# Kernel tuning notes

Measured on AMD Instinct MI355X. Metric: run time of the kernel, lower is better.

## Reference

```python
import jax, jax.numpy as jnp
import numpy as np

B, A, C_CLS = 64, 9, 20
H_FEAT, W_FEAT = 28, 28
IN_DIM, HID = 1280, 128
N_GT, M_POS = 40, 2048
AC5 = 5 * A + C_CLS


def setup_inputs() -> dict:
    key = jax.random.key(0)
    ks = jax.random.split(key, 10)
    features = jax.random.normal(ks[0], (B, IN_DIM, H_FEAT, W_FEAT), jnp.float32)
    # valid GT boxes in feature-map coordinates: (x1, y1, x2, y2, class)
    x1 = jax.random.uniform(ks[1], (B, N_GT), minval=0.0, maxval=W_FEAT - 6.0)
    y1 = jax.random.uniform(ks[2], (B, N_GT), minval=0.0, maxval=H_FEAT - 6.0)
    bw = jax.random.uniform(ks[3], (B, N_GT), minval=1.0, maxval=5.0)
    bh = jax.random.uniform(ks[4], (B, N_GT), minval=1.0, maxval=5.0)
    cls = jax.random.randint(ks[5], (B, N_GT), 0, C_CLS).astype(jnp.float32)
    bboxes = jnp.stack([x1, y1, x1 + bw, y1 + bh, cls], axis=-1)
    n_anchors_total = B * A * H_FEAT * W_FEAT
    pos_anchor_idx = jax.random.randint(ks[6], (M_POS,), 0, n_anchors_total, dtype=jnp.int32)
    neg_anchor_idx = jax.random.randint(ks[7], (M_POS,), 0, n_anchors_total, dtype=jnp.int32)
    W1 = jax.random.normal(ks[8], (HID, IN_DIM), jnp.float32) * 0.02
    b1 = jnp.zeros((HID,), jnp.float32)
    W2 = jax.random.normal(ks[9], (AC5, HID), jnp.float32) * 0.02
    b2 = jnp.zeros((AC5,), jnp.float32)
    anc = jnp.array([[1.0, 1], [2, 2], [3, 3], [4, 4], [5, 5], [2, 3], [3, 2], [3, 5], [5, 3]], jnp.float32)
    return dict(features=features, bboxes=bboxes, pos_anchor_idx=pos_anchor_idx,
                neg_anchor_idx=neg_anchor_idx, W1=W1, b1=b1, W2=W2, b2=b2, anc=anc)


def _detector_loss(features, bboxes, pos_idx, neg_idx, W1, b1, W2, b2, anc):
    Bx, _, Hf, Wf = features.shape
    N = bboxes.shape[1]
    Mp = pos_idx.shape[0]
    # ---- prediction network: two 1x1 convs (dropout skipped: eval mode) ----
    h = jnp.einsum('bchw,oc->bohw', features, W1) + b1[None, :, None, None]
    h = jax.nn.leaky_relu(h, 0.01)
    x = jnp.einsum('bchw,oc->bohw', h, W2) + b2[None, :, None, None]
    x_anchor = x[:, :5 * A].reshape(Bx, A, 5, Hf, Wf)  # (B,A,5,H,W)
    x_class = x[:, 5 * A:]                              # (B,C,H,W)
    # ---- GenerateGrid + GenerateAnchor ----
    xs = jnp.arange(Wf, dtype=jnp.float32) + 0.5
    ys = jnp.arange(Hf, dtype=jnp.float32) + 0.5
    gx, gy = jnp.meshgrid(xs, ys, indexing='xy')        # both (H,W)
    grid = jnp.stack([gx, gy], axis=-1)                 # (H,W,2)
    half = anc / 2.0                                    # (A,2)
    tl = grid[None] - half[:, None, None]               # (A,H,W,2)
    br = grid[None] + half[:, None, None]
    anchors = jnp.concatenate([tl, br], axis=-1)        # (A,H,W,4)
    p = jnp.broadcast_to(anchors[None], (Bx, A, Hf, Wf, 4)).reshape(Bx, -1, 4)  # (B,M,4)
    # ---- IoU matrix (B, M, N), exactly as source (signed w*h -> positive area) ----
    area_p = ((p[..., 0] - p[..., 2]) * (p[..., 1] - p[..., 3]))[:, :, None]
    area_b = ((bboxes[..., 2] - bboxes[..., 0]) * (bboxes[..., 3] - bboxes[..., 1]))[:, None, :]
    ix1 = jnp.maximum(p[:, :, None, 0], bboxes[:, None, :, 0])
    iy1 = jnp.maximum(p[:, :, None, 1], bboxes[:, None, :, 1])
    ix2 = jnp.minimum(p[:, :, None, 2], bboxes[:, None, :, 2])
    iy2 = jnp.minimum(p[:, :, None, 3], bboxes[:, None, :, 3])
    inter = jnp.clip(ix2 - ix1, 0.0) * jnp.clip(iy2 - iy1, 0.0)
    iou_mat = inter / (area_p + area_b - inter)          # (B,M,N)
    # ---- gather-based anchor/class extraction ----
    anc_data = jnp.transpose(x_anchor, (0, 1, 3, 4, 2)).reshape(-1, 5)  # (B*A*H*W, 5)
    pos_a = anc_data[pos_idx]
    neg_a = anc_data[neg_idx]
    conf_scores = jax.nn.sigmoid(jnp.concatenate([pos_a[:, 0], neg_a[:, 0]])[:, None])  # (2M,1)
    off = pos_a[:, 1:]
    offsets = jnp.concatenate([jax.nn.sigmoid(off[:, :2]) - 0.5, off[:, 2:]], axis=1)   # (M,4)
    cls_all = jnp.transpose(x_class, (0, 2, 3, 1))                       # (B,H,W,C)
    cls_all = jnp.broadcast_to(cls_all[:, None], (Bx, A, Hf, Wf, C_CLS)).reshape(-1, C_CLS)
    class_scores = cls_all[pos_idx]                                      # (M,C)
    # ---- match positives to GT via IoU argmax, build GT offsets/classes ----
    Mflat = A * Hf * Wf
    bpos = pos_idx // Mflat
    mpos = pos_idx % Mflat
    iou_pos = iou_mat[bpos, mpos]                 # (M,N)
    matched = jnp.argmax(iou_pos, axis=1)         # (M,)
    gt_box = bboxes[bpos, matched]                # (M,5)
    a_box = p[bpos, mpos]                         # (M,4)
    xa = 0.5 * (a_box[:, 0] + a_box[:, 2]); ya = 0.5 * (a_box[:, 1] + a_box[:, 3])
    wa = a_box[:, 2] - a_box[:, 0];          ha = a_box[:, 3] - a_box[:, 1]
    xb = 0.5 * (gt_box[:, 0] + gt_box[:, 2]); yb = 0.5 * (gt_box[:, 1] + gt_box[:, 3])
    wb = gt_box[:, 2] - gt_box[:, 0];          hb = gt_box[:, 3] - gt_box[:, 1]
    gt_offsets = jnp.stack([xb - xa, yb - ya, jnp.log(wb / wa), jnp.log(hb / ha)], axis=1)
    gt_offsets = jax.lax.stop_gradient(gt_offsets)
    gt_cls = gt_box[:, 4].astype(jnp.int32)
    # ---- losses (w_conf = w_reg = w_cls = 1) ----
    gt_conf = jnp.concatenate([jnp.ones((Mp, 1), jnp.float32), jnp.zeros((Mp, 1), jnp.float32)], axis=0)
    conf_loss = jnp.sum((conf_scores - gt_conf) ** 2) / (2.0 * Mp)
    reg_loss = jnp.sum((offsets - gt_offsets) ** 2) / Mp
    logp = jax.nn.log_softmax(class_scores, axis=-1)
    cls_loss = -jnp.mean(jnp.take_along_axis(logp, gt_cls[:, None], axis=1))
    return conf_loss + reg_loss + cls_loss


def reference(features, bboxes, pos_anchor_idx, neg_anchor_idx, W1, b1, W2, b2, anc):
    return _detector_loss(features, bboxes, pos_anchor_idx, neg_anchor_idx, W1, b1, W2, b2, anc)
```

## Files before the change

kernel.cpp:

```cpp
#include <hip/hip_runtime.h>
#include <math.h>

#define NPOS   2048
#define NANCH  4096
#define CIN    1280
#define HID    128
#define W_     28
#define HW_    784
#define AHW    7056
#define FB     (CIN*HW_)
#define SLAB   8
#define SLABF  (SLAB*HW_)
#define SLABP  6400

__device__ __forceinline__ float sigmoidf_(float x) {
    return 1.0f / (1.0f + __expf(-x));
}
__device__ __forceinline__ unsigned short f2bf(float x) {
    unsigned int u = __float_as_uint(x);
    return (unsigned short)((u + 0x7fffu + ((u >> 16) & 1u)) >> 16);
}
__device__ __forceinline__ float bf_lo(unsigned int w) { return __uint_as_float(w << 16); }
__device__ __forceinline__ float bf_hi(unsigned int w) { return __uint_as_float(w & 0xffff0000u); }

typedef __attribute__((address_space(3))) float lds_f;
typedef __attribute__((address_space(1))) const float glb_f;
__device__ __forceinline__ void gload16(const float* g, float* l) {
    __builtin_amdgcn_global_load_lds((glb_f*)g, (lds_f*)l, 16, 0, 0);
}

__global__ __launch_bounds__(256, 2) void k_fused(
    const float* __restrict__ F, const float* __restrict__ W1,
    const int* __restrict__ posi, const int* __restrict__ negi,
    unsigned short* __restrict__ Hp, int kchunk, int nslab)
{
    __shared__ float Pl[2][SLABP];
    __shared__ float Wl[2][SLAB][4][32];
    __shared__ float Gl[SLAB][128];
    __shared__ int   hwl[128];
    __shared__ int   gll[128];
    __shared__ int   nbL;

    const int b    = blockIdx.x;
    const int ks   = blockIdx.y;
    const int t    = threadIdx.x;
    const int w    = t >> 6;
    const int lane = t & 63;

    if (t == 0) nbL = 0;
    if (t < 128) hwl[t] = 0;
    __syncthreads();
#pragma unroll
    for (int r = 0; r < 16; ++r) {
        const int g    = r * 256 + t;
        const int aidx = (g < NPOS) ? posi[g] : negi[g - NPOS];
        const int bb   = aidx / AHW;
        if (bb == b) {
            const int hw   = (aidx - bb * AHW) % HW_;
            const int slot = atomicAdd(&nbL, 1);
            if (slot < 128) { hwl[slot] = hw; gll[slot] = g; }
        }
    }
    __syncthreads();
    const int nb = nbL;

    const bool wact = (w * 32) < nb;
    const int  i2   = lane >> 1;
    const int  hh   = lane & 1;
    const int  s_g  = w * 32 + i2;
    const int  a0   = w * 32 + (lane & 15) * 2;
    const int  og   = lane >> 4;

    float4 acc[2][8];
#pragma unroll
    for (int ai = 0; ai < 2; ++ai)
#pragma unroll
        for (int j = 0; j < 8; ++j) acc[ai][j] = make_float4(0.f, 0.f, 0.f, 0.f);

    const int kb0 = ks * kchunk;
    const int o_w = t >> 1, q_w = t & 1;

    {
        const float* src = F + (size_t)b * FB + (size_t)kb0 * HW_;
        for (int c = w; c < 24; c += 4)
            gload16(src + c * 256 + lane * 4, &Pl[0][c * 256]);
        if (w == 0 && lane < 32)
            gload16(src + 6144 + lane * 4, &Pl[0][6144]);
        const float4 wv = *(const float4*)&W1[(size_t)o_w * CIN + kb0 + 4 * q_w];
        Wl[0][4 * q_w + 0][o_w >> 5][o_w & 31] = wv.x;
        Wl[0][4 * q_w + 1][o_w >> 5][o_w & 31] = wv.y;
        Wl[0][4 * q_w + 2][o_w >> 5][o_w & 31] = wv.z;
        Wl[0][4 * q_w + 3][o_w >> 5][o_w & 31] = wv.w;
    }
    __syncthreads();

    int cur = 0;
    for (int sl = 0; sl < nslab; ++sl) {
        if (sl + 1 < nslab) {
            const int kb = kb0 + (sl + 1) * SLAB;
            const float* src = F + (size_t)b * FB + (size_t)kb * HW_;
            float* dst = &Pl[cur ^ 1][0];
            for (int c = w; c < 24; c += 4)
                gload16(src + c * 256 + lane * 4, dst + c * 256);
            if (w == 0 && lane < 32)
                gload16(src + 6144 + lane * 4, dst + 6144);
            const float4 wv = *(const float4*)&W1[(size_t)o_w * CIN + kb + 4 * q_w];
            Wl[cur ^ 1][4 * q_w + 0][o_w >> 5][o_w & 31] = wv.x;
            Wl[cur ^ 1][4 * q_w + 1][o_w >> 5][o_w & 31] = wv.y;
            Wl[cur ^ 1][4 * q_w + 2][o_w >> 5][o_w & 31] = wv.z;
            Wl[cur ^ 1][4 * q_w + 3][o_w >> 5][o_w & 31] = wv.w;
        }
        if (wact) {
            const int hw = hwl[s_g];
#pragma unroll
            for (int c = 0; c < 4; ++c)
                Gl[4 * hh + c][s_g] = Pl[cur][(4 * hh + c) * HW_ + hw];
#pragma unroll
            for (int kk = 0; kk < SLAB; ++kk) {
                const float2 g2 = *(const float2*)&Gl[kk][a0];
#pragma unroll
                for (int j = 0; j < 8; ++j) {
                    const float4 wv = *(const float4*)&Wl[cur][kk][og][4 * j];
                    acc[0][j].x = fmaf(g2.x, wv.x, acc[0][j].x);
                    acc[0][j].y = fmaf(g2.x, wv.y, acc[0][j].y);
                    acc[0][j].z = fmaf(g2.x, wv.z, acc[0][j].z);
                    acc[0][j].w = fmaf(g2.x, wv.w, acc[0][j].w);
                    acc[1][j].x = fmaf(g2.y, wv.x, acc[1][j].x);
                    acc[1][j].y = fmaf(g2.y, wv.y, acc[1][j].y);
                    acc[1][j].z = fmaf(g2.y, wv.z, acc[1][j].z);
                    acc[1][j].w = fmaf(g2.y, wv.w, acc[1][j].w);
                }
            }
        }
        __syncthreads();
        cur ^= 1;
    }

    if (wact) {
#pragma unroll
        for (int ai = 0; ai < 2; ++ai) {
            const int s = a0 + ai;
            if (s < nb) {
                const int g = gll[s];
                unsigned short* dst = Hp + ((size_t)ks * NANCH + g) * HID + og * 32;
                unsigned int u[16];
#pragma unroll
                for (int j = 0; j < 8; ++j) {
                    u[2 * j]     = (unsigned)f2bf(acc[ai][j].x) |
                                   ((unsigned)f2bf(acc[ai][j].y) << 16);
                    u[2 * j + 1] = (unsigned)f2bf(acc[ai][j].z) |
                                   ((unsigned)f2bf(acc[ai][j].w) << 16);
                }
#pragma unroll
                for (int q = 0; q < 4; ++q)
                    *(uint4*)(dst + 8 * q) =
                        make_uint4(u[4 * q], u[4 * q + 1], u[4 * q + 2], u[4 * q + 3]);
            }
        }
    }
}

__global__ __launch_bounds__(256) void k_loss(
    const unsigned short* __restrict__ Hp, const float* __restrict__ b1,
    int ksel, const float* __restrict__ W2, const float* __restrict__ b2,
    const int* __restrict__ posi, const int* __restrict__ negi,
    const float* __restrict__ bboxes, const float* __restrict__ anc,
    float* __restrict__ contrib)
{
    const int wid  = threadIdx.x >> 6;
    const int lane = threadIdx.x & 63;
    const int g    = blockIdx.x * 4 + wid;

    const int aidx = (g < NPOS) ? posi[g] : negi[g - NPOS];
    const int b   = aidx / AHW;
    const int rem = aidx - b * AHW;
    const int a   = rem / HW_;
    const int hw  = rem - a * HW_;
    const int hh  = hw / W_;
    const int ww  = hw - hh * W_;

    float hx = b1[2 * lane], hy = b1[2 * lane + 1];
    for (int ks = 0; ks < ksel; ++ks) {
        const unsigned raw =
            *(const unsigned*)&Hp[((size_t)ks * NANCH + g) * HID + 2 * lane];
        hx += bf_lo(raw);
        hy += bf_hi(raw);
    }
    hx = (hx > 0.0f) ? hx : 0.01f * hx;
    hy = (hy > 0.0f) ? hy : 0.01f * hy;

    if (g < NPOS) {
        float outv[25];
#pragma unroll
        for (int j = 0; j < 25; ++j) {
            const int row = (j < 5) ? (5 * a + j) : (40 + j);
            const float2 w = *(const float2*)&W2[(size_t)row * HID + 2 * lane];
            float v = fmaf(w.x, hx, w.y * hy);
#pragma unroll
            for (int off = 1; off < 64; off <<= 1) v += __shfl_xor(v, off, 64);
            outv[j] = v + b2[row];
        }

        const float wa = anc[2 * a], ha = anc[2 * a + 1];
        const float cx = ww + 0.5f, cy = hh + 0.5f;
        const float ax1 = cx - 0.5f * wa, ay1 = cy - 0.5f * ha;
        const float ax2 = cx + 0.5f * wa, ay2 = cy + 0.5f * ha;
        const float areap = wa * ha;

        float v; int vi = lane;
        if (lane < 40) {
            const float* bb = &bboxes[(size_t)(b * 40 + lane) * 5];
            const float bx1 = bb[0], by1 = bb[1], bx2 = bb[2], by2 = bb[3];
            const float areab = (bx2 - bx1) * (by2 - by1);
            const float ix1 = fmaxf(ax1, bx1), iy1 = fmaxf(ay1, by1);
            const float ix2 = fminf(ax2, bx2), iy2 = fminf(ay2, by2);
            const float inter = fmaxf(ix2 - ix1, 0.0f) * fmaxf(iy2 - iy1, 0.0f);
            v = inter / (areap + areab - inter);
        } else {
            v = -1.0f;
        }
#pragma unroll
        for (int off = 1; off < 64; off <<= 1) {
            const float ov = __shfl_xor(v, off, 64);
            const int   oi = __shfl_xor(vi, off, 64);
            if (ov > v || (ov == v && oi < vi)) { v = ov; vi = oi; }
        }
        const int m = vi;

        const float* gt = &bboxes[(size_t)(b * 40 + m) * 5];
        const float gx1 = gt[0], gy1 = gt[1], gx2 = gt[2], gy2 = gt[3];
        const int   gcls = (int)gt[4];
        const float xb = 0.5f * (gx1 + gx2), yb = 0.5f * (gy1 + gy2);
        const float wb = gx2 - gx1, hb = gy2 - gy1;
        const float go0 = xb - cx, go1 = yb - cy;
        const float go2 = __logf(wb / wa), go3 = __logf(hb / ha);

        const float o0 = sigmoidf_(outv[1]) - 0.5f;
        const float o1 = sigmoidf_(outv[2]) - 0.5f;
        const float o2 = outv[3], o3 = outv[4];
        const float reg = (o0 - go0) * (o0 - go0) + (o1 - go1) * (o1 - go1) +
                          (o2 - go2) * (o2 - go2) + (o3 - go3) * (o3 - go3);

        const float conf = sigmoidf_(outv[0]);
        const float conft = (conf - 1.0f) * (conf - 1.0f);

        float mx = outv[5];
#pragma unroll
        for (int c = 1; c < 20; ++c) mx = fmaxf(mx, outv[5 + c]);
        float se = 0.0f;
#pragma unroll
        for (int c = 0; c < 20; ++c) se += __expf(outv[5 + c] - mx);
        float lgt = 0.0f;
#pragma unroll
        for (int c = 0; c < 20; ++c) if (c == gcls) lgt = outv[5 + c];
        const float clst = -(lgt - mx - __logf(se));

        if (lane == 0)
            contrib[g] = conft * (1.0f / 4096.0f) + reg * (1.0f / 2048.0f) +
                         clst * (1.0f / 2048.0f);
    } else {
        const int row = 5 * a;
        const float2 w = *(const float2*)&W2[(size_t)row * HID + 2 * lane];
        float v = fmaf(w.x, hx, w.y * hy);
#pragma unroll
        for (int off = 1; off < 64; off <<= 1) v += __shfl_xor(v, off, 64);
        const float conf = sigmoidf_(v + b2[row]);
        if (lane == 0) contrib[g] = conf * conf * (1.0f / 4096.0f);
    }
}

__global__ __launch_bounds__(256) void k_final(const float* __restrict__ contrib,
                                               float* __restrict__ out)
{
    __shared__ float red[256];
    const int t = threadIdx.x;
    float s = 0.0f;
    for (int i = t; i < NANCH; i += 256) s += contrib[i];
    red[t] = s;
    __syncthreads();
    for (int st = 128; st > 0; st >>= 1) {
        if (t < st) red[t] += red[t + st];
        __syncthreads();
    }
    if (t == 0) out[0] = red[0];
}

extern "C" void kernel_launch(void* const* d_in, const int* in_sizes, int n_in,
                              void* d_out, int out_size, void* d_ws, size_t ws_size,
                              hipStream_t stream)
{
    const float* F      = (const float*)d_in[0];
    const float* bboxes = (const float*)d_in[1];
    const int*   posi   = (const int*)d_in[2];
    const int*   negi   = (const int*)d_in[3];
    const float* W1     = (const float*)d_in[4];
    const float* b1     = (const float*)d_in[5];
    const float* W2     = (const float*)d_in[6];
    const float* b2     = (const float*)d_in[7];
    const float* anc    = (const float*)d_in[8];
    float* out = (float*)d_out;

    char* ws = (char*)d_ws;
    int KSEL = 4;
    {
        const int opts[2] = {8, 4};
        for (int i = 0; i < 2; ++i) {
            size_t need = (size_t)opts[i] * NANCH * HID * 2 + (size_t)NANCH * 4 + 256;
            if (need <= ws_size) { KSEL = opts[i]; break; }
        }
    }
    unsigned short* Hp      = (unsigned short*)ws;
    float*          contrib = (float*)(ws + (size_t)KSEL * NANCH * HID * 2);

    const int kchunk = CIN / KSEL;
    const int nslab  = kchunk / SLAB;

    k_fused<<<dim3(64, KSEL), 256, 0, stream>>>(F, W1, posi, negi, Hp,
                                                kchunk, nslab);
    k_loss<<<NANCH / 4, 256, 0, stream>>>(Hp, b1, KSEL, W2, b2, posi, negi,
                                          bboxes, anc, contrib);
    k_final<<<1, 256, 0, stream>>>(contrib, out);
    (void)in_sizes; (void)n_in; (void)out_size;
}
```

Before: 86.28 us.

## Triple-stage async slab prefetch with explicit vmcnt waits and DMA-loaded W1

Restructures the gather-GEMM pipeline so that two slabs of features and weights are kept in flight using global_load_lds. Completion is tracked with manual s_waitcnt vmcnt and raw s_barrier in place of __syncthreads. W1 is now loaded straight into LDS through the same async path, in a padded row-major layout, instead of being transposed through registers. The gathered tile is stored anchor-major with zero padding for rows past the valid count. Anchor index and hw are packed into one int. The aim is to hide global latency and cut sync overhead, at the cost of fragile hand-tuned wait counts and changed LDS bank patterns.

```diff
diff --git a/kernel.cpp b/kernel.cpp
--- a/kernel.cpp
+++ b/kernel.cpp
@@ -11,7 +11,6 @@
 #define FB     (CIN*HW_)
 #define SLAB   8
 #define SLABF  (SLAB*HW_)
-#define SLABP  6400
 
 __device__ __forceinline__ float sigmoidf_(float x) {
     return 1.0f / (1.0f + __expf(-x));
@@ -28,17 +27,22 @@
 __device__ __forceinline__ void gload16(const float* g, float* l) {
     __builtin_amdgcn_global_load_lds((glb_f*)g, (lds_f*)l, 16, 0, 0);
 }
+
+#define SCHED_FENCE() __builtin_amdgcn_sched_barrier(0)
+#define WAIT_VM8()  asm volatile("s_waitcnt vmcnt(8)" ::: "memory")
+#define WAIT_VM7()  asm volatile("s_waitcnt vmcnt(7)" ::: "memory")
+#define WAIT_VM0()  asm volatile("s_waitcnt vmcnt(0)" ::: "memory")
+#define WAIT_LGKM0() asm volatile("s_waitcnt lgkmcnt(0)" ::: "memory")
 
 __global__ __launch_bounds__(256, 2) void k_fused(
     const float* __restrict__ F, const float* __restrict__ W1,
     const int* __restrict__ posi, const int* __restrict__ negi,
     unsigned short* __restrict__ Hp, int kchunk, int nslab)
 {
-    __shared__ float Pl[2][SLABP];
-    __shared__ float Wl[2][SLAB][4][32];
-    __shared__ float Gl[SLAB][128];
-    __shared__ int   hwl[128];
-    __shared__ int   gll[128];
+    __shared__ float Pl[2][SLABF];
+    __shared__ float Wl[2][1040];
+    __shared__ float Gl[128][8];
+    __shared__ int   pkl[128];
     __shared__ int   nbL;
 
     const int b    = blockIdx.x;
@@ -48,7 +52,7 @@
     const int lane = t & 63;
 
     if (t == 0) nbL = 0;
-    if (t < 128) hwl[t] = 0;
+    if (t < 128) pkl[t] = 0;
     __syncthreads();
 #pragma unroll
     for (int r = 0; r < 16; ++r) {
@@ -58,82 +62,101 @@
         if (bb == b) {
             const int hw   = (aidx - bb * AHW) % HW_;
             const int slot = atomicAdd(&nbL, 1);
-            if (slot < 128) { hwl[slot] = hw; gll[slot] = g; }
+            if (slot < 128) pkl[slot] = (g << 10) | hw;
         }
     }
     __syncthreads();
     const int nb = nbL;
 
     const bool wact = (w * 32) < nb;
-    const int  i2   = lane >> 1;
+    const int  s_g  = w * 32 + (lane >> 1);
     const int  hh   = lane & 1;
-    const int  s_g  = w * 32 + i2;
     const int  a0   = w * 32 + (lane & 15) * 2;
     const int  og   = lane >> 4;
 
-    float4 acc[2][8];
+    float acc[2][32];
 #pragma unroll
     for (int ai = 0; ai < 2; ++ai)
 #pragma unroll
-        for (int j = 0; j < 8; ++j) acc[ai][j] = make_float4(0.f, 0.f, 0.f, 0.f);
+        for (int o = 0; o < 32; ++o) acc[ai][o] = 0.0f;
 
     const int kb0 = ks * kchunk;
-    const int o_w = t >> 1, q_w = t & 1;
-
-    {
-        const float* src = F + (size_t)b * FB + (size_t)kb0 * HW_;
-        for (int c = w; c < 24; c += 4)
-            gload16(src + c * 256 + lane * 4, &Pl[0][c * 256]);
+
+    auto issue = [&](int sl2, int buf) {
+        const int kb = kb0 + sl2 * SLAB;
+        const float* srcP = F + (size_t)b * FB + (size_t)kb * HW_;
+        float* dstP = &Pl[buf][0];
+#pragma unroll
+        for (int i = 0; i < 6; ++i) {
+            const int c = w + 4 * i;
+            gload16(srcP + c * 256 + lane * 4, dstP + c * 256);
+        }
         if (w == 0 && lane < 32)
-            gload16(src + 6144 + lane * 4, &Pl[0][6144]);
-        const float4 wv = *(const float4*)&W1[(size_t)o_w * CIN + kb0 + 4 * q_w];
-        Wl[0][4 * q_w + 0][o_w >> 5][o_w & 31] = wv.x;
-        Wl[0][4 * q_w + 1][o_w >> 5][o_w & 31] = wv.y;
-        Wl[0][4 * q_w + 2][o_w >> 5][o_w & 31] = wv.z;
-        Wl[0][4 * q_w + 3][o_w >> 5][o_w & 31] = wv.w;
-    }
-    __syncthreads();
-
-    int cur = 0;
+            gload16(srcP + 6144 + lane * 4, dstP + 6144);
+        gload16(W1 + (size_t)(w * 32 + (lane >> 1)) * CIN + kb + 4 * (lane & 1),
+                &Wl[buf][w * 260]);
+    };
+
+    issue(0, 0);
+    issue(1, 1);
+    SCHED_FENCE();
+    if (w == 0) { WAIT_VM8(); } else { WAIT_VM7(); }
+    SCHED_FENCE();
+    __builtin_amdgcn_s_barrier();
+    SCHED_FENCE();
+
     for (int sl = 0; sl < nslab; ++sl) {
-        if (sl + 1 < nslab) {
-            const int kb = kb0 + (sl + 1) * SLAB;
-            const float* src = F + (size_t)b * FB + (size_t)kb * HW_;
-            float* dst = &Pl[cur ^ 1][0];
-            for (int c = w; c < 24; c += 4)
-                gload16(src + c * 256 + lane * 4, dst + c * 256);
-            if (w == 0 && lane < 32)
-                gload16(src + 6144 + lane * 4, dst + 6144);
-            const float4 wv = *(const float4*)&W1[(size_t)o_w * CIN + kb + 4 * q_w];
-            Wl[cur ^ 1][4 * q_w + 0][o_w >> 5][o_w & 31] = wv.x;
-            Wl[cur ^ 1][4 * q_w + 1][o_w >> 5][o_w & 31] = wv.y;
-            Wl[cur ^ 1][4 * q_w + 2][o_w >> 5][o_w & 31] = wv.z;
-            Wl[cur ^ 1][4 * q_w + 3][o_w >> 5][o_w & 31] = wv.w;
-        }
+        const int cur = sl & 1;
         if (wact) {
-            const int hw = hwl[s_g];
-#pragma unroll
-            for (int c = 0; c < 4; ++c)
-                Gl[4 * hh + c][s_g] = Pl[cur][(4 * hh + c) * HW_ + hw];
-#pragma unroll
-            for (int kk = 0; kk < SLAB; ++kk) {
-                const float2 g2 = *(const float2*)&Gl[kk][a0];
-#pragma unroll
-                for (int j = 0; j < 8; ++j) {
-                    const float4 wv = *(const float4*)&Wl[cur][kk][og][4 * j];
-                    acc[0][j].x = fmaf(g2.x, wv.x, acc[0][j].x);
-                    acc[0][j].y = fmaf(g2.x, wv.y, acc[0][j].y);
-                    acc[0][j].z = fmaf(g2.x, wv.z, acc[0][j].z);
-                    acc[0][j].w = fmaf(g2.x, wv.w, acc[0][j].w);
-                    acc[1][j].x = fmaf(g2.y, wv.x, acc[1][j].x);
-                    acc[1][j].y = fmaf(g2.y, wv.y, acc[1][j].y);
-                    acc[1][j].z = fmaf(g2.y, wv.z, acc[1][j].z);
-                    acc[1][j].w = fmaf(g2.y, wv.w, acc[1][j].w);
+            const int  pk   = pkl[s_g];
+            const int  hw   = pk & 1023;
+            const bool real = (s_g < nb);
+#pragma unroll
+            for (int c = 0; c < 4; ++c) {
+                const float v = Pl[cur][(4 * hh + c) * HW_ + hw];
+                Gl[s_g][4 * hh + c] = real ? v : 0.0f;
+            }
+            const float4 gA0 = *(const float4*)&Gl[a0][0];
+            const float4 gB0 = *(const float4*)&Gl[a0][4];
+            const float4 gA1 = *(const float4*)&Gl[a0 + 1][0];
+            const float4 gB1 = *(const float4*)&Gl[a0 + 1][4];
+            const float* wbase = &Wl[cur][og * 260];
+#pragma unroll
+            for (int j = 0; j < 8; ++j) {
+#pragma unroll
+                for (int c = 0; c < 4; ++c) {
+                    const int ol = 4 * j + c;
+                    const float4 wA = *(const float4*)&wbase[ol * 8];
+                    const float4 wB = *(const float4*)&wbase[ol * 8 + 4];
+                    float v0 = acc[0][ol], v1 = acc[1][ol];
+                    v0 = fmaf(gA0.x, wA.x, v0); v1 = fmaf(gA1.x, wA.x, v1);
+                    v0 = fmaf(gA0.y, wA.y, v0); v1 = fmaf(gA1.y, wA.y, v1);
+                    v0 = fmaf(gA0.z, wA.z, v0); v1 = fmaf(gA1.z, wA.z, v1);
+                    v0 = fmaf(gA0.w, wA.w, v0); v1 = fmaf(gA1.w, wA.w, v1);
+                    v0 = fmaf(gB0.x, wB.x, v0); v1 = fmaf(gB1.x, wB.x, v1);
+                    v0 = fmaf(gB0.y, wB.y, v0); v1 = fmaf(gB1.y, wB.y, v1);
+                    v0 = fmaf(gB0.z, wB.z, v0); v1 = fmaf(gB1.z, wB.z, v1);
+                    v0 = fmaf(gB0.w, wB.w, v0); v1 = fmaf(gB1.w, wB.w, v1);
+                    acc[0][ol] = v0; acc[1][ol] = v1;
                 }
             }
         }
-        __syncthreads();
-        cur ^= 1;
+        if (sl + 1 < nslab) {
+            WAIT_LGKM0();
+            SCHED_FENCE();
+            __builtin_amdgcn_s_barrier();
+            SCHED_FENCE();
+            if (sl + 2 < nslab) {
+                issue(sl + 2, cur);
+                SCHED_FENCE();
+                if (w == 0) { WAIT_VM8(); } else { WAIT_VM7(); }
+            } else {
+                WAIT_VM0();
+            }
+            SCHED_FENCE();
+            __builtin_amdgcn_s_barrier();
+            SCHED_FENCE();
+        }
     }
 
     if (wact) {
@@ -141,16 +164,13 @@
         for (int ai = 0; ai < 2; ++ai) {
             const int s = a0 + ai;
             if (s < nb) {
-                const int g = gll[s];
+                const int g = pkl[s] >> 10;
                 unsigned short* dst = Hp + ((size_t)ks * NANCH + g) * HID + og * 32;
                 unsigned int u[16];
 #pragma unroll
-                for (int j = 0; j < 8; ++j) {
-                    u[2 * j]     = (unsigned)f2bf(acc[ai][j].x) |
-                                   ((unsigned)f2bf(acc[ai][j].y) << 16);
-                    u[2 * j + 1] = (unsigned)f2bf(acc[ai][j].z) |
-                                   ((unsigned)f2bf(acc[ai][j].w) << 16);
-                }
+                for (int q = 0; q < 16; ++q)
+                    u[q] = (unsigned)f2bf(acc[ai][2 * q]) |
+                           ((unsigned)f2bf(acc[ai][2 * q + 1]) << 16);
 #pragma unroll
                 for (int q = 0; q < 4; ++q)
                     *(uint4*)(dst + 8 * q) =
```

After: 85.96 us. About the same (-0.4%).
